# Kernel tuning notes

Hardware: AMD Instinct MI355X
Metric: run time of the kernel (lower is better)

The kernel has to match this reference:

```python
import jax, jax.numpy as jnp
import numpy as np

N, M, D = 32768, 4096, 32


def setup_inputs() -> dict:
    key = jax.random.key(0)
    k1, k2, k3 = jax.random.split(key, 3)
    X = jax.random.normal(k1, (N, D), dtype=jnp.float32)
    centers = jax.random.normal(k2, (M, D), dtype=jnp.float32)
    # fitted Nystrom coefficients (params from .fit); b = Vj(1) in the Genred formula
    alphas = jax.random.normal(k3, (M, 1), dtype=jnp.float32) * 0.05
    sigma = jnp.ones((1,), dtype=jnp.float32)  # Pm(1) kernel lengthscale g
    return {"X": X, "centers": centers, "alphas": alphas, "sigma": sigma}


def reference(X, centers, alphas, sigma):
    # Genred formula: Exp(SqDist(x/g, y/g) * IntInv(-2)) * b, reduced over j (axis=1)
    g = sigma[0]
    xs = X / g           # [N, D]
    ys = centers / g     # [M, D]
    x2 = jnp.sum(xs * xs, axis=1, keepdims=True)            # [N, 1]
    y2 = jnp.sum(ys * ys, axis=1, keepdims=True).T          # [1, M]
    sqdist = x2 + y2 - 2.0 * (xs @ ys.T)                    # [N, M]
    k = jnp.exp(-0.5 * sqdist)                              # RBF kernel values
    return k @ alphas                                       # [N, 1]
```

## Files before the change

### kernel.cpp

```cpp
#include <hip/hip_runtime.h>

#define NN 32768
#define MM 4096
#define DD 32

typedef short short8 __attribute__((ext_vector_type(8)));
typedef float f32x4 __attribute__((ext_vector_type(4)));

#define ROWTILES 2
#define WAVES 4

__device__ __forceinline__ unsigned short f2bf(float f) {
    unsigned u = __float_as_uint(f);
    unsigned r = 0x7FFFu + ((u >> 16) & 1u);
    return (unsigned short)((u + r) >> 16);
}
__device__ __forceinline__ float bf2f(unsigned short h) {
    return __uint_as_float(((unsigned)h) << 16);
}

__global__ __launch_bounds__(256) void prep_kern(
    const float* __restrict__ X, const float* __restrict__ C,
    const float* __restrict__ alphas, const float* __restrict__ sigma,
    unsigned short* __restrict__ Xh, unsigned short* __restrict__ Xl,
    unsigned short* __restrict__ Ch, unsigned short* __restrict__ Cl,
    float* __restrict__ Bx, float* __restrict__ w)
{
    int i = blockIdx.x * 256 + threadIdx.x;
    float g = sigma[0];
    float LA = 1.44269504088896340736f / (g * g);

    const float* src;
    unsigned short* dh;
    unsigned short* dl;
    int row;
    bool isX = (i < NN);
    if (isX) {
        row = i;
        src = X + (size_t)row * DD;
        dh = Xh + (size_t)row * DD;
        dl = Xl + (size_t)row * DD;
    } else {
        row = i - NN;
        if (row >= MM) return;
        src = C + (size_t)row * DD;
        dh = Ch + (size_t)row * DD;
        dl = Cl + (size_t)row * DD;
    }
    const float scale = isX ? LA : 1.0f;

    float s2 = 0.f;
#pragma unroll
    for (int q = 0; q < DD / 8; ++q) {
        float4 a = ((const float4*)src)[2 * q];
        float4 b = ((const float4*)src)[2 * q + 1];
        float vv[8] = {a.x, a.y, a.z, a.w, b.x, b.y, b.z, b.w};
        short8 hv, lv;
#pragma unroll
        for (int e = 0; e < 8; ++e) {
            float v = vv[e];
            s2 = fmaf(v, v, s2);
            float sv = v * scale;
            unsigned short h = f2bf(sv);
            hv[e] = (short)h;
            lv[e] = (short)f2bf(sv - bf2f(h));
        }
        ((short8*)dh)[q] = hv;
        ((short8*)dl)[q] = lv;
    }
    float b = -0.5f * LA * s2;
    if (isX) Bx[row] = b;
    else     w[row] = alphas[row] * exp2f(b);
}

template <int MS>
__global__ __launch_bounds__(256, 8) void rbf_mfma_lds(
    const unsigned short* __restrict__ Xh, const unsigned short* __restrict__ Xl,
    const unsigned short* __restrict__ Ch, const unsigned short* __restrict__ Cl,
    const float* __restrict__ Bx, const float* __restrict__ w,
    float* __restrict__ part)
{
    constexpr int MPER = MM / MS;
    constexpr int NT = MPER / 16;
    __shared__ unsigned short sCh[MPER * DD];
    __shared__ unsigned short sCl[MPER * DD];
    __shared__ float sw[MPER];

    const int tid = threadIdx.x;
    const int wave = tid >> 6;
    const int lane = tid & 63;
    const int l15 = lane & 15;
    const int lhi = lane >> 4;
    const int rowbase = (blockIdx.x * WAVES + wave) * (16 * ROWTILES);
    const int slice = blockIdx.y;
    const int j0 = slice * MPER;

    {
        const float4* gh = (const float4*)(Ch + (size_t)j0 * DD);
        const float4* gl = (const float4*)(Cl + (size_t)j0 * DD);
        float4* lh = (float4*)sCh;
        float4* ll = (float4*)sCl;
        constexpr int NV = MPER * DD / 8;
#pragma unroll
        for (int o = tid; o < NV; o += 256) {
            lh[o] = gh[o];
            ll[o] = gl[o];
        }
        if (tid < MPER) sw[tid] = w[j0 + tid];
    }

    short8 ah[ROWTILES], al[ROWTILES];
#pragma unroll
    for (int t = 0; t < ROWTILES; ++t) {
        int r = rowbase + t * 16 + l15;
        ah[t] = *(const short8*)(Xh + (size_t)r * DD + lhi * 8);
        al[t] = *(const short8*)(Xl + (size_t)r * DD + lhi * 8);
    }
    f32x4 bx[ROWTILES];
#pragma unroll
    for (int t = 0; t < ROWTILES; ++t) {
        float4 v = *(const float4*)&Bx[rowbase + t * 16 + lhi * 4];
        bx[t][0] = v.x; bx[t][1] = v.y; bx[t][2] = v.z; bx[t][3] = v.w;
    }

    f32x4 acc[ROWTILES];
#pragma unroll
    for (int t = 0; t < ROWTILES; ++t) acc[t] = (f32x4){0.f, 0.f, 0.f, 0.f};

    __syncthreads();

#pragma unroll 2
    for (int jt = 0; jt < NT; ++jt) {
        const int r = jt * 16 + l15;
        short8 bh = *(const short8*)&sCh[r * DD + lhi * 8];
        short8 bl = *(const short8*)&sCl[r * DD + lhi * 8];
        float wj = sw[r];
#pragma unroll
        for (int t = 0; t < ROWTILES; ++t) {
            f32x4 d = bx[t];
            d = __builtin_amdgcn_mfma_f32_16x16x32_bf16(ah[t], bl, d, 0, 0, 0);
            d = __builtin_amdgcn_mfma_f32_16x16x32_bf16(al[t], bh, d, 0, 0, 0);
            d = __builtin_amdgcn_mfma_f32_16x16x32_bf16(ah[t], bh, d, 0, 0, 0);
#pragma unroll
            for (int rr = 0; rr < 4; ++rr)
                acc[t][rr] = fmaf(wj, __builtin_amdgcn_exp2f(d[rr]), acc[t][rr]);
        }
    }

#pragma unroll
    for (int t = 0; t < ROWTILES; ++t)
#pragma unroll
        for (int rr = 0; rr < 4; ++rr) {
            float v = acc[t][rr];
            v += __shfl_xor(v, 1, 64);
            v += __shfl_xor(v, 2, 64);
            v += __shfl_xor(v, 4, 64);
            v += __shfl_xor(v, 8, 64);
            acc[t][rr] = v;
        }
    if (l15 == 0) {
#pragma unroll
        for (int t = 0; t < ROWTILES; ++t)
            *(f32x4*)&part[(size_t)slice * NN + rowbase + t * 16 + lhi * 4] = acc[t];
    }
}

template <int MS>
__global__ __launch_bounds__(256) void reduce_kern(const float* __restrict__ part,
                                                   float* __restrict__ out) {
    int i = blockIdx.x * 256 + threadIdx.x;
    float s = 0.f;
#pragma unroll
    for (int k = 0; k < MS; ++k) s += part[(size_t)k * NN + i];
    out[i] = s;
}

__global__ __launch_bounds__(256) void wkern(const float* __restrict__ C,
                                             const float* __restrict__ alphas,
                                             const float* __restrict__ sigma,
                                             float* __restrict__ w) {
    int j = blockIdx.x * 256 + threadIdx.x;
    if (j >= MM) return;
    float g = sigma[0];
    float inv_g2 = 1.0f / (g * g);
    const float4* cp = (const float4*)(C + (size_t)j * DD);
    float y2 = 0.f;
#pragma unroll
    for (int q = 0; q < DD / 4; ++q) {
        float4 v = cp[q];
        y2 = fmaf(v.x, v.x, y2);
        y2 = fmaf(v.y, v.y, y2);
        y2 = fmaf(v.z, v.z, y2);
        y2 = fmaf(v.w, v.w, y2);
    }
    w[j] = alphas[j] * exp2f(-0.5f * inv_g2 * 1.44269504088896340736f * y2);
}

__global__ __launch_bounds__(128) void rbf_valu(const float* __restrict__ X,
                                                const float* __restrict__ C,
                                                const float* __restrict__ w,
                                                const float* __restrict__ sigma,
                                                float* __restrict__ out) {
    const int row = blockIdx.x * 128 + threadIdx.x;
    const float g = sigma[0];
    const float A = 1.44269504088896340736f / (g * g);
    float x[DD];
    const float4* xp = (const float4*)(X + (size_t)row * DD);
#pragma unroll
    for (int q = 0; q < DD / 4; ++q) {
        float4 v = xp[q];
        x[4 * q + 0] = v.x; x[4 * q + 1] = v.y;
        x[4 * q + 2] = v.z; x[4 * q + 3] = v.w;
    }
    float x2 = 0.f;
#pragma unroll
    for (int d = 0; d < DD; ++d) x2 = fmaf(x[d], x[d], x2);
    const float B = -0.5f * A * x2;
    float acc = 0.f;
#pragma unroll 2
    for (int j = 0; j < MM; ++j) {
        const float* cj = C + (size_t)j * DD;
        float d0 = 0.f, d1 = 0.f, d2 = 0.f, d3 = 0.f;
#pragma unroll
        for (int d = 0; d < DD; d += 4) {
            d0 = fmaf(cj[d + 0], x[d + 0], d0);
            d1 = fmaf(cj[d + 1], x[d + 1], d1);
            d2 = fmaf(cj[d + 2], x[d + 2], d2);
            d3 = fmaf(cj[d + 3], x[d + 3], d3);
        }
        float dot = (d0 + d1) + (d2 + d3);
        acc = fmaf(w[j], exp2f(fmaf(dot, A, B)), acc);
    }
    out[row] = acc;
}

extern "C" void kernel_launch(void* const* d_in, const int* in_sizes, int n_in,
                              void* d_out, int out_size, void* d_ws, size_t ws_size,
                              hipStream_t stream) {
    const float* X  = (const float*)d_in[0];
    const float* C  = (const float*)d_in[1];
    const float* al = (const float*)d_in[2];
    const float* sg = (const float*)d_in[3];
    float* out = (float*)d_out;

    size_t off = 0;
    unsigned short* Xh = (unsigned short*)((char*)d_ws + off); off += (size_t)NN * DD * 2;
    unsigned short* Xl = (unsigned short*)((char*)d_ws + off); off += (size_t)NN * DD * 2;
    unsigned short* Ch = (unsigned short*)((char*)d_ws + off); off += (size_t)MM * DD * 2;
    unsigned short* Cl = (unsigned short*)((char*)d_ws + off); off += (size_t)MM * DD * 2;
    float* Bx = (float*)((char*)d_ws + off); off += (size_t)NN * 4;
    float* w  = (float*)((char*)d_ws + off); off += (size_t)MM * 4;
    float* part = (float*)((char*)d_ws + off);
    const size_t base = off;

    const size_t need32 = base + (size_t)32 * NN * 4;
    const size_t need8  = base + (size_t)8 * NN * 4;

    if (ws_size >= need8) {
        prep_kern<<<(NN + MM) / 256, 256, 0, stream>>>(X, C, al, sg, Xh, Xl, Ch, Cl, Bx, w);
        if (ws_size >= need32) {
            dim3 grid(NN / (WAVES * 16 * ROWTILES), 32);
            rbf_mfma_lds<32><<<grid, 64 * WAVES, 0, stream>>>(Xh, Xl, Ch, Cl, Bx, w, part);
            reduce_kern<32><<<NN / 256, 256, 0, stream>>>(part, out);
        } else {
            dim3 grid(NN / (WAVES * 16 * ROWTILES), 8);
            rbf_mfma_lds<8><<<grid, 64 * WAVES, 0, stream>>>(Xh, Xl, Ch, Cl, Bx, w, part);
            reduce_kern<8><<<NN / 256, 256, 0, stream>>>(part, out);
        }
    } else {
        float* wf = (float*)d_ws;
        wkern<<<MM / 256, 256, 0, stream>>>(C, al, sg, wf);
        rbf_valu<<<NN / 128, 128, 0, stream>>>(X, C, wf, sg, out);
    }
}
```

Measured before the change: 42.56 us.

## Double row tiles per wave, swizzle LDS centers, prefetch next B fragment

Each wave now handles four 16-row tiles instead of two, so every center fragment read from LDS feeds more MFMAs, and occupancy hints drop to 4 blocks per SM to leave room for the extra registers. Center data in LDS is stored with an XOR swizzle to avoid bank conflicts on the strided 16-byte fragment reads. The next iteration's B fragment and weight are loaded before the current MFMAs run, to hide LDS latency. The risks are lower occupancy, a grid half as large (fewer blocks to spread across CUs), and higher register pressure.

```diff
diff --git a/kernel.cpp b/kernel.cpp
--- a/kernel.cpp
+++ b/kernel.cpp
@@ -7,7 +7,7 @@
 typedef short short8 __attribute__((ext_vector_type(8)));
 typedef float f32x4 __attribute__((ext_vector_type(4)));
 
-#define ROWTILES 2
+#define ROWTILES 4
 #define WAVES 4
 
 __device__ __forceinline__ unsigned short f2bf(float f) {
@@ -74,7 +74,7 @@
 }
 
 template <int MS>
-__global__ __launch_bounds__(256, 8) void rbf_mfma_lds(
+__global__ __launch_bounds__(256, 4) void rbf_mfma_lds(
     const unsigned short* __restrict__ Xh, const unsigned short* __restrict__ Xl,
     const unsigned short* __restrict__ Ch, const unsigned short* __restrict__ Cl,
     const float* __restrict__ Bx, const float* __restrict__ w,
@@ -95,16 +95,18 @@
     const int slice = blockIdx.y;
     const int j0 = slice * MPER;
 
+    char* lh = (char*)sCh;
+    char* ll = (char*)sCl;
+
     {
         const float4* gh = (const float4*)(Ch + (size_t)j0 * DD);
         const float4* gl = (const float4*)(Cl + (size_t)j0 * DD);
-        float4* lh = (float4*)sCh;
-        float4* ll = (float4*)sCl;
         constexpr int NV = MPER * DD / 8;
 #pragma unroll
         for (int o = tid; o < NV; o += 256) {
-            lh[o] = gh[o];
-            ll[o] = gl[o];
+            int b = 16 * (o ^ ((o >> 2) & 7));
+            *(float4*)(lh + b) = gh[o];
+            *(float4*)(ll + b) = gl[o];
         }
         if (tid < MPER) sw[tid] = w[j0 + tid];
     }
@@ -129,12 +131,25 @@
 
     __syncthreads();
 
+    short8 bh, bl;
+    float wj;
+    {
+        int b = (l15 * 64 + lhi * 16) ^ ((l15 & 7) << 4);
+        bh = *(const short8*)(lh + b);
+        bl = *(const short8*)(ll + b);
+        wj = sw[l15];
+    }
 #pragma unroll 2
     for (int jt = 0; jt < NT; ++jt) {
-        const int r = jt * 16 + l15;
-        short8 bh = *(const short8*)&sCh[r * DD + lhi * 8];
-        short8 bl = *(const short8*)&sCl[r * DD + lhi * 8];
-        float wj = sw[r];
+        short8 nbh = bh, nbl = bl;
+        float nwj = wj;
+        if (jt + 1 < NT) {
+            int r = (jt + 1) * 16 + l15;
+            int b = (r * 64 + lhi * 16) ^ ((r & 7) << 4);
+            nbh = *(const short8*)(lh + b);
+            nbl = *(const short8*)(ll + b);
+            nwj = sw[r];
+        }
 #pragma unroll
         for (int t = 0; t < ROWTILES; ++t) {
             f32x4 d = bx[t];
@@ -145,6 +160,7 @@
             for (int rr = 0; rr < 4; ++rr)
                 acc[t][rr] = fmaf(wj, __builtin_amdgcn_exp2f(d[rr]), acc[t][rr]);
         }
+        bh = nbh; bl = nbl; wj = nwj;
     }
 
 #pragma unroll
```

After: 40.00 us. 6.0% less time.
